# Kernel tuning notes

Hardware: AMD Instinct MI355X
Metric: run time of the kernel (lower is better)

The kernel has to match this reference:

```python
import jax, jax.numpy as jnp
import numpy as np

B, S, HID = 2, 2048, 2048
NH, NKV, HD = 16, 4, 128
GROUPS = NH // NKV
CLIP = 8.0
ROPE_THETA = 500000.0
QKV_OUT = HID + 2 * NKV * HD  # 3072
NEG = jnp.finfo(jnp.float32).min


def setup_inputs() -> dict:
    key = jax.random.key(0)
    k1, k2, k3 = jax.random.split(key, 3)
    hidden_states = jax.random.normal(k1, (B, S, HID), dtype=jnp.float32)
    position_ids = jnp.tile(jnp.arange(S, dtype=jnp.int64)[None, :], (B, 1))
    Wqkv = jax.random.normal(k2, (QKV_OUT, HID), dtype=jnp.float32) * (HID ** -0.5)
    Wout = jax.random.normal(k3, (HID, HID), dtype=jnp.float32) * (HID ** -0.5)
    return {"hidden_states": hidden_states, "position_ids": position_ids,
            "Wqkv": Wqkv, "Wout": Wout}


def _rotate_half(x):
    x1, x2 = jnp.split(x, 2, axis=-1)
    return jnp.concatenate((-x2, x1), axis=-1)


def reference(hidden_states, position_ids, Wqkv, Wout):
    b, s, _ = hidden_states.shape
    # fused QKV projection + clamp
    qkv = jnp.einsum('bsh,oh->bso', hidden_states, Wqkv)
    qkv = jnp.clip(qkv, -CLIP, CLIP)
    q, k, v = jnp.split(qkv, [HID, HID + NKV * HD], axis=2)
    q = q.reshape(b, s, NH, HD).transpose(0, 2, 1, 3)   # [b, nh, s, hd]
    k = k.reshape(b, s, NKV, HD).transpose(0, 2, 1, 3)  # [b, nkv, s, hd]
    v = v.reshape(b, s, NKV, HD).transpose(0, 2, 1, 3)
    # rotary embedding
    inv_freq = 1.0 / (ROPE_THETA ** (jnp.arange(0, HD, 2, dtype=jnp.float32) / HD))
    freqs = position_ids.astype(jnp.float32)[:, :, None] * inv_freq[None, None, :]  # [b,s,hd/2]
    emb = jnp.concatenate((freqs, freqs), axis=-1)      # [b, s, hd]
    cos = jnp.cos(emb)[:, None, :, :]                   # [b, 1, s, hd]
    sin = jnp.sin(emb)[:, None, :, :]
    q = q * cos + _rotate_half(q) * sin
    k = k * cos + _rotate_half(k) * sin
    # repeat kv heads (GQA)
    k = jnp.repeat(k, GROUPS, axis=1)  # [b, nh, s, hd]
    v = jnp.repeat(v, GROUPS, axis=1)
    # attention with additive causal mask
    scores = jnp.einsum('bhqd,bhkd->bhqk', q, k) / jnp.sqrt(jnp.float32(HD))
    causal = jnp.where(jnp.tril(jnp.ones((s, s), dtype=bool)), 0.0, NEG)
    scores = scores + causal[None, None, :, :]
    attn = jax.nn.softmax(scores.astype(jnp.float32), axis=-1).astype(q.dtype)
    out = jnp.einsum('bhqk,bhkd->bhqd', attn, v)
    out = out.transpose(0, 2, 1, 3).reshape(b, s, HID)
    return jnp.einsum('bsh,oh->bso', out, Wout)
```

## Files before the change

kernel.cpp:

```cpp
#include <hip/hip_runtime.h>
#include <stdint.h>

#define S_    2048
#define HID_  2048
#define NH_   16
#define NKV_  4
#define HD_   128

using short4x = __attribute__((ext_vector_type(4))) short;
using short8  = __attribute__((ext_vector_type(8))) short;
using floatx4 = __attribute__((ext_vector_type(4))) float;

#define NEGBIG (-3.0e38f)

__device__ __forceinline__ unsigned short f2bf(float x) {
  union { float f; unsigned u; } v; v.f = x;
  unsigned r = v.u + 0x7fffu + ((v.u >> 16) & 1u);
  return (unsigned short)(r >> 16);
}
__device__ __forceinline__ float bf2f(unsigned short b) {
  union { unsigned u; float f; } v; v.u = ((unsigned)b) << 16;
  return v.f;
}
__device__ __forceinline__ void ld_lds16(const void* g, void* l) {
  __builtin_amdgcn_global_load_lds(
      (const __attribute__((address_space(1))) unsigned*)g,
      (__attribute__((address_space(3))) unsigned*)l, 16, 0, 0);
}

__global__ void k_cvt3(const float* __restrict__ s0, unsigned short* __restrict__ d0, int n0,
                       const float* __restrict__ s1, unsigned short* __restrict__ d1, int n1,
                       const float* __restrict__ s2, unsigned short* __restrict__ d2, int n2) {
  int i = blockIdx.x * blockDim.x + threadIdx.x;
  const float* s; unsigned short* d;
  if (i < n0) { s = s0; d = d0; }
  else if (i < n0 + n1) { s = s1; d = d1; i -= n0; }
  else { s = s2; d = d2; i -= n0 + n1; if (i >= n2) return; }
  float4 v = ((const float4*)s)[i];
  union { unsigned short us[4]; uint2 u2; } u;
  u.us[0] = f2bf(v.x); u.us[1] = f2bf(v.y); u.us[2] = f2bf(v.z); u.us[3] = f2bf(v.w);
  ((uint2*)d)[i] = u.u2;
}

__global__ void k_rope2(unsigned short* __restrict__ Qb, unsigned short* __restrict__ Kb,
                        const int* __restrict__ pos, int nQ, float qscale) {
  int idx = blockIdx.x * blockDim.x + threadIdx.x;
  unsigned short* buf; int nh; float oscale;
  if (idx < nQ) { buf = Qb; nh = NH_; oscale = qscale; }
  else { buf = Kb; nh = NKV_; oscale = 1.0f; idx -= nQ; }
  int d = idx & 63;
  int h = (idx >> 6) % nh;
  int m = idx / (unsigned)(nh << 6);
  float p = (float)pos[m];
  float inv = expf(-(float)d * (13.122363377404328f / 64.0f));
  float f = p * inv;
  float cs = cosf(f), sn = sinf(f);
  size_t base = (size_t)m * (nh * HD_) + h * HD_ + d;
  float x1 = bf2f(buf[base]), x2 = bf2f(buf[base + 64]);
  buf[base]      = f2bf((x1 * cs - x2 * sn) * oscale);
  buf[base + 64] = f2bf((x2 * cs + x1 * sn) * oscale);
}

template <int EPI>
__global__ void __launch_bounds__(256)
k_gemm_bt(const unsigned short* __restrict__ A, const unsigned short* __restrict__ Bw,
          unsigned short* __restrict__ Qb, unsigned short* __restrict__ Kb,
          unsigned short* __restrict__ Vt, float* __restrict__ Of) {
  const int K = HID_;
  __shared__ __align__(16) unsigned short As[128 * 32];
  __shared__ __align__(16) unsigned short Bs[128 * 32];
  const int tid  = threadIdx.x;
  const int wave = tid >> 6, lane = tid & 63;
  const int quad = lane >> 4, l15 = lane & 15;
  const int wm = (wave >> 1) * 64, wn = (wave & 1) * 64;
  const int m0 = blockIdx.x * 128, n0 = blockIdx.y * 128;

  floatx4 acc[4][4] = {};

  const int srow = tid >> 2;
  const int scol = (tid & 3) * 8;
  const unsigned short* Ag0 = A  + (size_t)(m0 + srow)      * K + scol;
  const unsigned short* Ag1 = A  + (size_t)(m0 + 64 + srow) * K + scol;
  const unsigned short* Bg0 = Bw + (size_t)(n0 + srow)      * K + scol;
  const unsigned short* Bg1 = Bw + (size_t)(n0 + 64 + srow) * K + scol;
  unsigned short* lA0 = &As[tid * 8];
  unsigned short* lA1 = &As[2048 + tid * 8];
  unsigned short* lB0 = &Bs[tid * 8];
  unsigned short* lB1 = &Bs[2048 + tid * 8];

  for (int k0 = 0; k0 < K; k0 += 32) {
    __syncthreads();
    ld_lds16(Ag0 + k0, lA0);
    ld_lds16(Ag1 + k0, lA1);
    ld_lds16(Bg0 + k0, lB0);
    ld_lds16(Bg1 + k0, lB1);
    __syncthreads();
    short8 a[4], b[4];
#pragma unroll
    for (int i = 0; i < 4; i++) a[i] = *(const short8*)&As[(wm + i * 16 + l15) * 32 + quad * 8];
#pragma unroll
    for (int j = 0; j < 4; j++) b[j] = *(const short8*)&Bs[(wn + j * 16 + l15) * 32 + quad * 8];
#pragma unroll
    for (int i = 0; i < 4; i++)
#pragma unroll
      for (int j = 0; j < 4; j++)
        acc[i][j] = __builtin_amdgcn_mfma_f32_16x16x32_bf16(a[i], b[j], acc[i][j], 0, 0, 0);
  }

#pragma unroll
  for (int i = 0; i < 4; i++) {
#pragma unroll
    for (int j = 0; j < 4; j++) {
      const int col = n0 + wn + j * 16 + l15;
#pragma unroll
      for (int r = 0; r < 4; r++) {
        const int row = m0 + wm + i * 16 + quad * 4 + r;
        float x = acc[i][j][r];
        if (EPI == 0) {
          x = fminf(fmaxf(x, -8.0f), 8.0f);
          if (col < HID_) {
            Qb[(size_t)row * HID_ + col] = f2bf(x);
          } else if (col < HID_ + NKV_ * HD_) {
            Kb[(size_t)row * (NKV_ * HD_) + (col - HID_)] = f2bf(x);
          } else {
            int oo = col - (HID_ + NKV_ * HD_);
            int kvh = oo >> 7, d = oo & 127;
            int bb = row >> 11, ss = row & 2047;
            Vt[((size_t)((bb * NKV_ + kvh) * HD_ + d) << 11) + ss] = f2bf(x);
          }
        } else {
          Of[(size_t)row * HID_ + col] = x;
        }
      }
    }
  }
}

__global__ void __launch_bounds__(256, 2)
k_attn(const unsigned short* __restrict__ Qb, const unsigned short* __restrict__ Kb,
       const unsigned short* __restrict__ Vt, unsigned short* __restrict__ AO) {
  __shared__ __align__(16) unsigned short sm[2][16384];
  __shared__ __align__(16) unsigned short Pl[4][16][88];

  const int tid  = threadIdx.x;
  const int wave = tid >> 6, lane = tid & 63;
  const int quad = lane >> 4, l15 = lane & 15;
  const int tLow  = blockIdx.x;
  const int tHigh = 31 - tLow;
  const int q0L = tLow * 64, q0H = tHigh * 64;
  const int bh = blockIdx.y;
  const int b = bh >> 4, h = bh & 15;
  const int kvh = h >> 2;

  const int srow = tid >> 2;
  const int scolz = (((tid & 3) ^ ((tid >> 3) & 3)) * 8);
  const int qoff = ((quad ^ ((l15 >> 1) & 3)) * 8);

  {
    const unsigned short* qgL = Qb + (size_t)(b * S_ + q0L + srow) * HID_ + h * HD_ + scolz;
    const unsigned short* qgH = Qb + (size_t)(b * S_ + q0H + srow) * HID_ + h * HD_ + scolz;
#pragma unroll
    for (int i = 0; i < 4; i++) ld_lds16(qgL + i * 32, &sm[0][i * 2048 + tid * 8]);
#pragma unroll
    for (int i = 0; i < 4; i++) ld_lds16(qgH + i * 32, &sm[1][i * 2048 + tid * 8]);
  }
  __syncthreads();
  short8 qaL[4], qaH[4];
#pragma unroll
  for (int c = 0; c < 4; c++) {
    qaL[c] = *(const short8*)&sm[0][(c * 64 + wave * 16 + l15) * 32 + qoff];
    qaH[c] = *(const short8*)&sm[1][(c * 64 + wave * 16 + l15) * 32 + qoff];
  }
  __syncthreads();

  floatx4 oacL[8] = {}, oacH[8] = {};
  floatx4 oacEL = {}, oacEH = {};
  float mL = NEGBIG, mH = NEGBIG;

  const unsigned short* kgb = Kb + (size_t)b * S_ * (NKV_ * HD_) + kvh * HD_ + scolz;
  const unsigned short* vgb = Vt + (size_t)(b * NKV_ + kvh) * HD_ * S_;

  unsigned short* PlW = &Pl[wave][0][0];

  short8 ones;
#pragma unroll
  for (int i = 0; i < 8; i++) ones[i] = (short)0x3F80;

  auto stage = [&](int bufI, int j) {
    unsigned short* B = &sm[bufI][0];
    const unsigned short* kg = kgb + (size_t)(j * 64 + srow) * (NKV_ * HD_);
#pragma unroll
    for (int i = 0; i < 4; i++) ld_lds16(kg + i * 32, &B[i * 2048 + tid * 8]);
#pragma unroll
    for (int i = 0; i < 4; i++) {
      int c = i >> 1, rowd = (i & 1) * 64 + srow;
      ld_lds16(vgb + (size_t)rowd * S_ + j * 64 + c * 32 + scolz,
               &B[8192 + c * 4096 + (i & 1) * 2048 + tid * 8]);
    }
  };

  auto softmax_tile = [&](floatx4* sc, floatx4* oac, floatx4& oacE, float& m_run,
                          int q0, int j, bool diag, short8& pa0, short8& pa1) {
    if (diag) {
      const int rowq = q0 + wave * 16 + l15;
#pragma unroll
      for (int t = 0; t < 4; t++) {
        const int kb0 = j * 64 + t * 16 + quad * 4;
#pragma unroll
        for (int r = 0; r < 4; r++)
          if (kb0 + r > rowq) sc[t][r] = NEGBIG;
      }
    }
    float mx = sc[0][0];
#pragma unroll
    for (int t = 0; t < 4; t++)
#pragma unroll
      for (int r = 0; r < 4; r++) mx = fmaxf(mx, sc[t][r]);
    mx = fmaxf(mx, __shfl_xor(mx, 16));
    mx = fmaxf(mx, __shfl_xor(mx, 32));

    const float mo = m_run;
    m_run = fmaxf(mo, mx);
    if (__any(mx > mo)) {
      float alpha = __builtin_amdgcn_exp2f(mo - m_run);
      float al4[4];
#pragma unroll
      for (int r = 0; r < 4; r++) al4[r] = __shfl(alpha, quad * 4 + r, 16);
#pragma unroll
      for (int t = 0; t < 8; t++)
#pragma unroll
        for (int r = 0; r < 4; r++) oac[t][r] *= al4[r];
#pragma unroll
      for (int r = 0; r < 4; r++) oacE[r] *= al4[r];
    }
#pragma unroll
    for (int t = 0; t < 4; t++) {
      short4x pk;
#pragma unroll
      for (int r = 0; r < 4; r++)
        pk[r] = (short)f2bf(__builtin_amdgcn_exp2f(sc[t][r] - m_run));
      *(short4x*)&PlW[l15 * 88 + t * 16 + quad * 4] = pk;
    }
    pa0 = *(const short8*)&PlW[l15 * 88 + quad * 8];
    pa1 = *(const short8*)&PlW[l15 * 88 + 32 + quad * 8];
  };

  auto step_two = [&](int j, const unsigned short* Kt, const unsigned short* Vts,
                      bool diagL, bool diagH) {
    floatx4 scH[4] = {}, scL[4] = {};
#pragma unroll
    for (int t = 0; t < 4; t++)
#pragma unroll
      for (int c = 0; c < 4; c++) {
        short8 ka = *(const short8*)&Kt[c * 2048 + (t * 16 + l15) * 32 + qoff];
        scH[t] = __builtin_amdgcn_mfma_f32_16x16x32_bf16(ka, qaH[c], scH[t], 0, 0, 0);
        scL[t] = __builtin_amdgcn_mfma_f32_16x16x32_bf16(ka, qaL[c], scL[t], 0, 0, 0);
      }
    short8 paH0, paH1, paL0, paL1;
    softmax_tile(scH, oacH, oacEH, mH, q0H, j, diagH, paH0, paH1);
    softmax_tile(scL, oacL, oacEL, mL, q0L, j, diagL, paL0, paL1);
#pragma unroll
    for (int t = 0; t < 8; t++) {
      short8 vb0 = *(const short8*)&Vts[(t * 16 + l15) * 32 + qoff];
      oacH[t] = __builtin_amdgcn_mfma_f32_16x16x32_bf16(paH0, vb0, oacH[t], 0, 0, 0);
      oacL[t] = __builtin_amdgcn_mfma_f32_16x16x32_bf16(paL0, vb0, oacL[t], 0, 0, 0);
      short8 vb1 = *(const short8*)&Vts[4096 + (t * 16 + l15) * 32 + qoff];
      oacH[t] = __builtin_amdgcn_mfma_f32_16x16x32_bf16(paH1, vb1, oacH[t], 0, 0, 0);
      oacL[t] = __builtin_amdgcn_mfma_f32_16x16x32_bf16(paL1, vb1, oacL[t], 0, 0, 0);
    }
    oacEH = __builtin_amdgcn_mfma_f32_16x16x32_bf16(paH0, ones, oacEH, 0, 0, 0);
    oacEH = __builtin_amdgcn_mfma_f32_16x16x32_bf16(paH1, ones, oacEH, 0, 0, 0);
    oacEL = __builtin_amdgcn_mfma_f32_16x16x32_bf16(paL0, ones, oacEL, 0, 0, 0);
    oacEL = __builtin_amdgcn_mfma_f32_16x16x32_bf16(paL1, ones, oacEL, 0, 0, 0);
  };

  auto step_one = [&](int j, const unsigned short* Kt, const unsigned short* Vts, bool diagH) {
    floatx4 scH[4] = {};
#pragma unroll
    for (int t = 0; t < 4; t++)
#pragma unroll
      for (int c = 0; c < 4; c++) {
        short8 ka = *(const short8*)&Kt[c * 2048 + (t * 16 + l15) * 32 + qoff];
        scH[t] = __builtin_amdgcn_mfma_f32_16x16x32_bf16(ka, qaH[c], scH[t], 0, 0, 0);
      }
    short8 paH0, paH1;
    softmax_tile(scH, oacH, oacEH, mH, q0H, j, diagH, paH0, paH1);
#pragma unroll
    for (int t = 0; t < 8; t++) {
      short8 vb0 = *(const short8*)&Vts[(t * 16 + l15) * 32 + qoff];
      oacH[t] = __builtin_amdgcn_mfma_f32_16x16x32_bf16(paH0, vb0, oacH[t], 0, 0, 0);
      short8 vb1 = *(const short8*)&Vts[4096 + (t * 16 + l15) * 32 + qoff];
      oacH[t] = __builtin_amdgcn_mfma_f32_16x16x32_bf16(paH1, vb1, oacH[t], 0, 0, 0);
    }
    oacEH = __builtin_amdgcn_mfma_f32_16x16x32_bf16(paH0, ones, oacEH, 0, 0, 0);
    oacEH = __builtin_amdgcn_mfma_f32_16x16x32_bf16(paH1, ones, oacEH, 0, 0, 0);
  };

  stage(0, 0);
  int cur = 0;
  for (int j = 0; j <= tHigh; ++j) {
    __syncthreads();
    if (j < tHigh) stage(cur ^ 1, j + 1);
    const unsigned short* Kt  = &sm[cur][0];
    const unsigned short* Vts = Kt + 8192;
    if (j <= tLow) step_two(j, Kt, Vts, j == tLow, j == tHigh);
    else           step_one(j, Kt, Vts, j == tHigh);
    cur ^= 1;
  }

#pragma unroll
  for (int t = 0; t < 8; t++)
#pragma unroll
    for (int r = 0; r < 4; r++) {
      int rgL = q0L + wave * 16 + quad * 4 + r;
      int rgH = q0H + wave * 16 + quad * 4 + r;
      AO[(size_t)(b * S_ + rgL) * HID_ + h * HD_ + t * 16 + l15] = f2bf(oacL[t][r] / oacEL[r]);
      AO[(size_t)(b * S_ + rgH) * HID_ + h * HD_ + t * 16 + l15] = f2bf(oacH[t][r] / oacEH[r]);
    }
}

extern "C" void kernel_launch(void* const* d_in, const int* in_sizes, int n_in,
                              void* d_out, int out_size, void* d_ws, size_t ws_size,
                              hipStream_t stream) {
  (void)in_sizes; (void)n_in; (void)out_size; (void)ws_size;
  const float* hidden = (const float*)d_in[0];
  const int*   pos    = (const int*)d_in[1];
  const float* Wqkv   = (const float*)d_in[2];
  const float* Wout   = (const float*)d_in[3];
  float* out = (float*)d_out;

  unsigned short* ws = (unsigned short*)d_ws;
  const size_t M1 = 1024 * 1024;
  unsigned short* hb  = ws;
  unsigned short* wqb = ws + 8 * M1;
  unsigned short* wob = ws + 14 * M1;
  unsigned short* Qb  = ws + 18 * M1;
  unsigned short* Kb  = ws + 26 * M1;
  unsigned short* Vt  = ws + 28 * M1;
  unsigned short* AO  = hb;

  const float QSCL = 0.08838834764831845f * 1.4426950408889634f;
  const int nQrope = 2 * 2048 * NH_ * 64;
  const int nKrope = 2 * 2048 * NKV_ * 64;

  k_cvt3<<<18432, 256, 0, stream>>>(hidden, hb, 2097152,
                                    Wqkv, wqb, 1572864,
                                    Wout, wob, 1048576);
  k_gemm_bt<0><<<dim3(32, 24), 256, 0, stream>>>(hb, wqb, Qb, Kb, Vt, nullptr);
  k_rope2<<<(nQrope + nKrope) / 256, 256, 0, stream>>>(Qb, Kb, pos, nQrope, QSCL);
  k_attn<<<dim3(16, 32), 256, 0, stream>>>(Qb, Kb, Vt, AO);
  k_gemm_bt<1><<<dim3(32, 16), 256, 0, stream>>>(AO, wob, nullptr, nullptr, nullptr, out);
}
```

Baseline: 314.1 us.

## Replace GEMM with 256-row tiled, multi-stage pipelined, swizzled-LDS kernel

Replaces the 128x128 single-buffered bf16 GEMM with a 512-thread kernel using 256xBN tiles, a four-slot LDS ring prefetched two stages ahead, XOR-swizzled LDS addressing, workgroup-ID remapping for cache locality, and raised wave priority around the MFMA blocks. The goal is to hide global-load latency behind MFMA work, raise arithmetic intensity per tile and cut LDS bank conflicts in both projection GEMMs. The cost is a much larger LDS footprint and more registers, which limits occupancy. The hand-placed waitcnt and barrier sequencing adds synchronisation complexity, and the larger tiles give smaller grids that may leave CUs idle.

```diff
diff --git a/kernel.cpp b/kernel.cpp
--- a/kernel.cpp
+++ b/kernel.cpp
@@ -61,61 +61,108 @@
   buf[base + 64] = f2bf((x2 * cs + x1 * sn) * oscale);
 }
 
-template <int EPI>
-__global__ void __launch_bounds__(256)
-k_gemm_bt(const unsigned short* __restrict__ A, const unsigned short* __restrict__ Bw,
+template <int NREP, int EPI>
+__global__ void __launch_bounds__(512, 2)
+k_gemm256(const unsigned short* __restrict__ A, const unsigned short* __restrict__ Bw,
           unsigned short* __restrict__ Qb, unsigned short* __restrict__ Kb,
           unsigned short* __restrict__ Vt, float* __restrict__ Of) {
-  const int K = HID_;
-  __shared__ __align__(16) unsigned short As[128 * 32];
-  __shared__ __align__(16) unsigned short Bs[128 * 32];
+  constexpr int K  = HID_;
+  constexpr int NS = K / 32;
+  constexpr int BN = NREP * 64;
+  constexpr int LPS = 2 + BN / 128;
+
+  __shared__ __align__(16) unsigned short As[4][256 * 32];
+  __shared__ __align__(16) unsigned short Bs[4][BN * 32];
+
   const int tid  = threadIdx.x;
-  const int wave = tid >> 6, lane = tid & 63;
+  const int lane = tid & 63;
+  const int wid  = tid >> 6;
   const int quad = lane >> 4, l15 = lane & 15;
-  const int wm = (wave >> 1) * 64, wn = (wave & 1) * 64;
-  const int m0 = blockIdx.x * 128, n0 = blockIdx.y * 128;
-
-  floatx4 acc[4][4] = {};
-
-  const int srow = tid >> 2;
-  const int scol = (tid & 3) * 8;
-  const unsigned short* Ag0 = A  + (size_t)(m0 + srow)      * K + scol;
-  const unsigned short* Ag1 = A  + (size_t)(m0 + 64 + srow) * K + scol;
-  const unsigned short* Bg0 = Bw + (size_t)(n0 + srow)      * K + scol;
-  const unsigned short* Bg1 = Bw + (size_t)(n0 + 64 + srow) * K + scol;
-  unsigned short* lA0 = &As[tid * 8];
-  unsigned short* lA1 = &As[2048 + tid * 8];
-  unsigned short* lB0 = &Bs[tid * 8];
-  unsigned short* lB1 = &Bs[2048 + tid * 8];
-
-  for (int k0 = 0; k0 < K; k0 += 32) {
-    __syncthreads();
-    ld_lds16(Ag0 + k0, lA0);
-    ld_lds16(Ag1 + k0, lA1);
-    ld_lds16(Bg0 + k0, lB0);
-    ld_lds16(Bg1 + k0, lB1);
-    __syncthreads();
-    short8 a[4], b[4];
-#pragma unroll
-    for (int i = 0; i < 4; i++) a[i] = *(const short8*)&As[(wm + i * 16 + l15) * 32 + quad * 8];
-#pragma unroll
-    for (int j = 0; j < 4; j++) b[j] = *(const short8*)&Bs[(wn + j * 16 + l15) * 32 + quad * 8];
-#pragma unroll
-    for (int i = 0; i < 4; i++)
-#pragma unroll
-      for (int j = 0; j < 4; j++)
-        acc[i][j] = __builtin_amdgcn_mfma_f32_16x16x32_bf16(a[i], b[j], acc[i][j], 0, 0, 0);
+  const int wr = wid >> 2, wc = wid & 3;
+
+  const int gx = gridDim.x, gy = gridDim.y;
+  const int nwg = gx * gy;
+  const int lid = blockIdx.y * gx + blockIdx.x;
+  const int u = (lid & 7) * (nwg >> 3) + (lid >> 3);
+  const int by = u % gy;
+  const int bx = u / gy;
+  const int m0 = bx * 256, n0 = by * BN;
+
+  const int srow  = tid >> 2;
+  const int scolz = (((tid & 3) ^ ((tid >> 3) & 3)) * 8);
+  const int qoffz = ((quad ^ ((l15 >> 1) & 3)) * 8);
+
+  const unsigned short* Asrc = A  + (size_t)(m0 + srow) * K + scolz;
+  const unsigned short* Bsrc = Bw + (size_t)(n0 + srow) * K + scolz;
+
+  auto stageA = [&](int s) {
+    const int sl = s & 3;
+    const unsigned short* g = Asrc + s * 32;
+    ld_lds16(g, &As[sl][tid * 8]);
+    ld_lds16(g + (size_t)128 * K, &As[sl][4096 + tid * 8]);
+  };
+  auto stageB = [&](int s) {
+    const int sl = s & 3;
+    const unsigned short* g = Bsrc + s * 32;
+    ld_lds16(g, &Bs[sl][tid * 8]);
+    if (NREP == 4) ld_lds16(g + (size_t)128 * K, &Bs[sl][4096 + tid * 8]);
+  };
+
+  floatx4 acc[8][NREP] = {};
+
+  stageA(0); stageB(0); stageA(1); stageB(1);
+  asm volatile("s_waitcnt vmcnt(%0)" :: "n"(LPS) : "memory");
+  asm volatile("s_barrier" ::: "memory");
+
+  for (int s = 0; s < NS; ++s) {
+    const int sl = s & 3;
+    const bool pf = (s + 2 < NS);
+    short8 a[8], b[NREP];
+#pragma unroll
+    for (int m = 0; m < 8; ++m)
+      a[m] = *(const short8*)&As[sl][(wr * 128 + m * 16 + l15) * 32 + qoffz];
+#pragma unroll
+    for (int n = 0; n < 2; ++n)
+      b[n] = *(const short8*)&Bs[sl][(wc * (NREP * 16) + n * 16 + l15) * 32 + qoffz];
+    if (pf) stageA(s + 2);
+    if (NREP == 2 && pf) stageB(s + 2);
+    asm volatile("s_barrier" ::: "memory");
+    __builtin_amdgcn_s_setprio(1);
+#pragma unroll
+    for (int m = 0; m < 8; ++m)
+#pragma unroll
+      for (int n = 0; n < 2; ++n)
+        acc[m][n] = __builtin_amdgcn_mfma_f32_16x16x32_bf16(a[m], b[n], acc[m][n], 0, 0, 0);
+    __builtin_amdgcn_s_setprio(0);
+    asm volatile("s_barrier" ::: "memory");
+    if (NREP == 4) {
+#pragma unroll
+      for (int n = 2; n < 4; ++n)
+        b[n] = *(const short8*)&Bs[sl][(wc * 64 + n * 16 + l15) * 32 + qoffz];
+      if (pf) stageB(s + 2);
+      asm volatile("s_barrier" ::: "memory");
+      __builtin_amdgcn_s_setprio(1);
+#pragma unroll
+      for (int m = 0; m < 8; ++m)
+#pragma unroll
+        for (int n = 2; n < 4; ++n)
+          acc[m][n] = __builtin_amdgcn_mfma_f32_16x16x32_bf16(a[m], b[n], acc[m][n], 0, 0, 0);
+      __builtin_amdgcn_s_setprio(0);
+    }
+    if (pf) asm volatile("s_waitcnt vmcnt(%0)" :: "n"(LPS) : "memory");
+    else    asm volatile("s_waitcnt vmcnt(0)" ::: "memory");
+    asm volatile("s_barrier" ::: "memory");
   }
 
 #pragma unroll
-  for (int i = 0; i < 4; i++) {
-#pragma unroll
-    for (int j = 0; j < 4; j++) {
-      const int col = n0 + wn + j * 16 + l15;
-#pragma unroll
-      for (int r = 0; r < 4; r++) {
-        const int row = m0 + wm + i * 16 + quad * 4 + r;
-        float x = acc[i][j][r];
+  for (int m = 0; m < 8; ++m) {
+#pragma unroll
+    for (int n = 0; n < NREP; ++n) {
+      const int col = n0 + wc * (NREP * 16) + n * 16 + l15;
+#pragma unroll
+      for (int r = 0; r < 4; ++r) {
+        const int row = m0 + wr * 128 + m * 16 + quad * 4 + r;
+        float x = acc[m][n][r];
         if (EPI == 0) {
           x = fminf(fmaxf(x, -8.0f), 8.0f);
           if (col < HID_) {
@@ -346,8 +393,8 @@
   k_cvt3<<<18432, 256, 0, stream>>>(hidden, hb, 2097152,
                                     Wqkv, wqb, 1572864,
                                     Wout, wob, 1048576);
-  k_gemm_bt<0><<<dim3(32, 24), 256, 0, stream>>>(hb, wqb, Qb, Kb, Vt, nullptr);
+  k_gemm256<4, 0><<<dim3(16, 12), 512, 0, stream>>>(hb, wqb, Qb, Kb, Vt, nullptr);
   k_rope2<<<(nQrope + nKrope) / 256, 256, 0, stream>>>(Qb, Kb, pos, nQrope, QSCL);
   k_attn<<<dim3(16, 32), 256, 0, stream>>>(Qb, Kb, Vt, AO);
-  k_gemm_bt<1><<<dim3(32, 16), 256, 0, stream>>>(AO, wob, nullptr, nullptr, nullptr, out);
-}
+  k_gemm256<2, 1><<<dim3(16, 16), 512, 0, stream>>>(AO, wob, nullptr, nullptr, nullptr, out);
+}
```

Result: slower. 335.0 us (+6.7%).

## Replace GEMM with 8-wave double-buffered pipelined kernel using swizzled LDS

Applied to the files above, without the earlier changes.

Both projection GEMMs now use a new 512-thread kernel with 256xBN tiles, a K-step of 64, double-buffered LDS, and async global-to-LDS loads interleaved with MFMA phases using manual barriers and vmcnt waits. It adds an XOR swizzle on the LDS layout to avoid bank conflicts, a workgroup-id remap for cache locality, and s_setprio around MFMA bursts. The goal is to hide memory latency and raise MFMA utilization compared with the single-buffered 128x128 kernel that synchronized twice per 32-wide K step. In exchange it uses much more LDS and fewer blocks (192 and 256), and the hand-counted vmcnt values make correctness fragile.

```diff
diff --git a/kernel.cpp b/kernel.cpp
--- a/kernel.cpp
+++ b/kernel.cpp
@@ -27,6 +27,9 @@
       (const __attribute__((address_space(1))) unsigned*)g,
       (__attribute__((address_space(3))) unsigned*)l, 16, 0, 0);
 }
+
+#define BAR()  asm volatile("s_barrier" ::: "memory")
+#define WLDS() asm volatile("s_waitcnt lgkmcnt(0)" ::: "memory")
 
 __global__ void k_cvt3(const float* __restrict__ s0, unsigned short* __restrict__ d0, int n0,
                        const float* __restrict__ s1, unsigned short* __restrict__ d1, int n1,
@@ -61,61 +64,147 @@
   buf[base + 64] = f2bf((x2 * cs + x1 * sn) * oscale);
 }
 
-template <int EPI>
-__global__ void __launch_bounds__(256)
-k_gemm_bt(const unsigned short* __restrict__ A, const unsigned short* __restrict__ Bw,
-          unsigned short* __restrict__ Qb, unsigned short* __restrict__ Kb,
-          unsigned short* __restrict__ Vt, float* __restrict__ Of) {
-  const int K = HID_;
-  __shared__ __align__(16) unsigned short As[128 * 32];
-  __shared__ __align__(16) unsigned short Bs[128 * 32];
+template <int NREP, int EPI>
+__global__ void __launch_bounds__(512, 2)
+k_gemm8p(const unsigned short* __restrict__ A, const unsigned short* __restrict__ Bw,
+         unsigned short* __restrict__ Qb, unsigned short* __restrict__ Kb,
+         unsigned short* __restrict__ Vt, float* __restrict__ Of) {
+  constexpr int K  = HID_;
+  constexpr int NT = K / 64;
+  constexpr int BN = NREP * 64;
+
+  __shared__ __align__(16) unsigned short As[2][256 * 64];
+  __shared__ __align__(16) unsigned short Bs[2][BN * 64];
+
   const int tid  = threadIdx.x;
-  const int wave = tid >> 6, lane = tid & 63;
+  const int lane = tid & 63, wave = tid >> 6;
   const int quad = lane >> 4, l15 = lane & 15;
-  const int wm = (wave >> 1) * 64, wn = (wave & 1) * 64;
-  const int m0 = blockIdx.x * 128, n0 = blockIdx.y * 128;
-
-  floatx4 acc[4][4] = {};
-
-  const int srow = tid >> 2;
-  const int scol = (tid & 3) * 8;
-  const unsigned short* Ag0 = A  + (size_t)(m0 + srow)      * K + scol;
-  const unsigned short* Ag1 = A  + (size_t)(m0 + 64 + srow) * K + scol;
-  const unsigned short* Bg0 = Bw + (size_t)(n0 + srow)      * K + scol;
-  const unsigned short* Bg1 = Bw + (size_t)(n0 + 64 + srow) * K + scol;
-  unsigned short* lA0 = &As[tid * 8];
-  unsigned short* lA1 = &As[2048 + tid * 8];
-  unsigned short* lB0 = &Bs[tid * 8];
-  unsigned short* lB1 = &Bs[2048 + tid * 8];
-
-  for (int k0 = 0; k0 < K; k0 += 32) {
-    __syncthreads();
-    ld_lds16(Ag0 + k0, lA0);
-    ld_lds16(Ag1 + k0, lA1);
-    ld_lds16(Bg0 + k0, lB0);
-    ld_lds16(Bg1 + k0, lB1);
-    __syncthreads();
-    short8 a[4], b[4];
-#pragma unroll
-    for (int i = 0; i < 4; i++) a[i] = *(const short8*)&As[(wm + i * 16 + l15) * 32 + quad * 8];
-#pragma unroll
-    for (int j = 0; j < 4; j++) b[j] = *(const short8*)&Bs[(wn + j * 16 + l15) * 32 + quad * 8];
-#pragma unroll
-    for (int i = 0; i < 4; i++)
-#pragma unroll
-      for (int j = 0; j < 4; j++)
-        acc[i][j] = __builtin_amdgcn_mfma_f32_16x16x32_bf16(a[i], b[j], acc[i][j], 0, 0, 0);
+  const int wr = wave >> 2, wc = wave & 3;
+
+  const int gx = gridDim.x, gy = gridDim.y;
+  const int nwg = gx * gy;
+  const int lid = blockIdx.y * gx + blockIdx.x;
+  const int u = (lid & 7) * (nwg >> 3) + (lid >> 3);
+  const int by = u % gy, bx = u / gy;
+  const int m0 = bx * 256, n0 = by * BN;
+
+  const int scol = ((((tid >> 2) & 1) ^ ((tid >> 3) & 1)) * 32)
+                 + (((tid & 3) ^ ((tid >> 4) & 3)) * 8);
+  const int srow = tid >> 3;
+  const unsigned short* Ag = A  + (size_t)(m0 + srow) * K + scol;
+  const unsigned short* Bg = Bw + (size_t)(n0 + srow) * K + scol;
+
+  const int rks0 = (l15 & 1) * 32;
+  const int rks1 = rks0 ^ 32;
+  const int rsl  = (quad ^ ((l15 >> 1) & 3)) * 8;
+
+  auto stageA = [&](int t, int half) {
+    const int d = t & 1;
+    const unsigned short* g = Ag + (size_t)half * 128 * K + t * 64;
+    ld_lds16(g,                  &As[d][(half * 128) * 64 + tid * 8]);
+    ld_lds16(g + (size_t)64 * K, &As[d][(half * 128 + 64) * 64 + tid * 8]);
+  };
+  auto stageB = [&](int t, int half) {
+    const int d = t & 1;
+    const unsigned short* g = Bg + (size_t)half * 128 * K + t * 64;
+    ld_lds16(g,                  &Bs[d][(half * 128) * 64 + tid * 8]);
+    ld_lds16(g + (size_t)64 * K, &Bs[d][(half * 128 + 64) * 64 + tid * 8]);
+  };
+
+  floatx4 acc[8][NREP] = {};
+
+  auto ldA = [&](short8* a, int d, int mh) {
+#pragma unroll
+    for (int m = 0; m < 4; ++m) {
+      const int row = (mh * 4 + m) * 32 + wr * 16 + l15;
+      a[m * 2 + 0] = *(const short8*)&As[d][row * 64 + rks0 + rsl];
+      a[m * 2 + 1] = *(const short8*)&As[d][row * 64 + rks1 + rsl];
+    }
+  };
+  auto ldB = [&](short8* b, int d, int nh) {
+#pragma unroll
+    for (int n = 0; n < 2; ++n) {
+      const int row = (nh * 2 + n) * 64 + wc * 16 + l15;
+      b[n * 2 + 0] = *(const short8*)&Bs[d][row * 64 + rks0 + rsl];
+      b[n * 2 + 1] = *(const short8*)&Bs[d][row * 64 + rks1 + rsl];
+    }
+  };
+  auto mmac = [&](const short8* a, const short8* b, int mh, int nh) {
+    __builtin_amdgcn_s_setprio(1);
+#pragma unroll
+    for (int m = 0; m < 4; ++m)
+#pragma unroll
+      for (int n = 0; n < 2; ++n)
+#pragma unroll
+        for (int ks = 0; ks < 2; ++ks)
+          acc[mh * 4 + m][nh * 2 + n] = __builtin_amdgcn_mfma_f32_16x16x32_bf16(
+              a[m * 2 + ks], b[n * 2 + ks], acc[mh * 4 + m][nh * 2 + n], 0, 0, 0);
+    __builtin_amdgcn_s_setprio(0);
+  };
+
+  short8 a[8], b0[4], b1[4];
+
+  if (NREP == 4) {
+    stageA(0, 0); stageA(0, 1); stageB(0, 0); stageB(0, 1);
+    asm volatile("s_waitcnt vmcnt(4)" ::: "memory");
+    stageA(1, 0); stageB(1, 0); stageB(1, 1);
+    asm volatile("s_waitcnt vmcnt(6)" ::: "memory");
+    BAR();
+    for (int t = 0; t < NT; ++t) {
+      const int d = t & 1;
+      ldA(a, d, 0); ldB(b0, d, 0);
+      if (t + 1 < NT) stageA(t + 1, 1);
+      BAR(); WLDS();
+      mmac(a, b0, 0, 0);
+      BAR();
+      ldB(b1, d, 1);
+      if (t + 2 < NT) stageA(t + 2, 0);
+      BAR(); WLDS();
+      mmac(a, b1, 0, 1);
+      BAR();
+      ldA(a, d, 1);
+      if (t + 2 < NT) stageB(t + 2, 0);
+      BAR(); WLDS();
+      mmac(a, b1, 1, 1);
+      BAR();
+      if (t + 2 < NT) stageB(t + 2, 1);
+      mmac(a, b0, 1, 0);
+      if (t + 2 < NT) asm volatile("s_waitcnt vmcnt(6)" ::: "memory");
+      else            asm volatile("s_waitcnt vmcnt(0)" ::: "memory");
+      BAR();
+    }
+  } else {
+    stageA(0, 0); stageA(0, 1); stageB(0, 0);
+    asm volatile("s_waitcnt vmcnt(2)" ::: "memory");
+    stageA(1, 0); stageB(1, 0);
+    asm volatile("s_waitcnt vmcnt(4)" ::: "memory");
+    BAR();
+    for (int t = 0; t < NT; ++t) {
+      const int d = t & 1;
+      ldA(a, d, 0); ldB(b0, d, 0);
+      if (t + 1 < NT) stageA(t + 1, 1);
+      BAR(); WLDS();
+      mmac(a, b0, 0, 0);
+      BAR();
+      ldA(a, d, 1);
+      if (t + 2 < NT) { stageA(t + 2, 0); stageB(t + 2, 0); }
+      BAR(); WLDS();
+      mmac(a, b0, 1, 0);
+      if (t + 2 < NT) asm volatile("s_waitcnt vmcnt(4)" ::: "memory");
+      else            asm volatile("s_waitcnt vmcnt(0)" ::: "memory");
+      BAR();
+    }
   }
 
 #pragma unroll
-  for (int i = 0; i < 4; i++) {
-#pragma unroll
-    for (int j = 0; j < 4; j++) {
-      const int col = n0 + wn + j * 16 + l15;
-#pragma unroll
-      for (int r = 0; r < 4; r++) {
-        const int row = m0 + wm + i * 16 + quad * 4 + r;
-        float x = acc[i][j][r];
+  for (int mf = 0; mf < 8; ++mf) {
+#pragma unroll
+    for (int nf = 0; nf < NREP; ++nf) {
+      const int col = n0 + nf * 64 + wc * 16 + l15;
+#pragma unroll
+      for (int r = 0; r < 4; ++r) {
+        const int row = m0 + mf * 32 + wr * 16 + quad * 4 + r;
+        float x = acc[mf][nf][r];
         if (EPI == 0) {
           x = fminf(fmaxf(x, -8.0f), 8.0f);
           if (col < HID_) {
@@ -124,9 +213,9 @@
             Kb[(size_t)row * (NKV_ * HD_) + (col - HID_)] = f2bf(x);
           } else {
             int oo = col - (HID_ + NKV_ * HD_);
-            int kvh = oo >> 7, d = oo & 127;
+            int kvh = oo >> 7, d2 = oo & 127;
             int bb = row >> 11, ss = row & 2047;
-            Vt[((size_t)((bb * NKV_ + kvh) * HD_ + d) << 11) + ss] = f2bf(x);
+            Vt[((size_t)((bb * NKV_ + kvh) * HD_ + d2) << 11) + ss] = f2bf(x);
           }
         } else {
           Of[(size_t)row * HID_ + col] = x;
@@ -346,8 +435,8 @@
   k_cvt3<<<18432, 256, 0, stream>>>(hidden, hb, 2097152,
                                     Wqkv, wqb, 1572864,
                                     Wout, wob, 1048576);
-  k_gemm_bt<0><<<dim3(32, 24), 256, 0, stream>>>(hb, wqb, Qb, Kb, Vt, nullptr);
+  k_gemm8p<4, 0><<<dim3(16, 12), 512, 0, stream>>>(hb, wqb, Qb, Kb, Vt, nullptr);
   k_rope2<<<(nQrope + nKrope) / 256, 256, 0, stream>>>(Qb, Kb, pos, nQrope, QSCL);
   k_attn<<<dim3(16, 32), 256, 0, stream>>>(Qb, Kb, Vt, AO);
-  k_gemm_bt<1><<<dim3(32, 16), 256, 0, stream>>>(AO, wob, nullptr, nullptr, nullptr, out);
-}
+  k_gemm8p<2, 1><<<dim3(16, 16), 512, 0, stream>>>(AO, wob, nullptr, nullptr, nullptr, out);
+}
```

Result: slower. 338.7 us (+7.8%).

## Fuse RoPE into QKV GEMM epilogue and defer softmax rescale by threshold

Applied to the files above, without the earlier changes.

The separate rotary-embedding kernel is removed and RoPE plus the Q scale are applied in the QKV GEMM epilogue. Each wave's clamped accumulators are exchanged through shared memory so that partner halves (d and d+64) can be rotated together. Q/K tiles are now written once, which avoids a full read-modify-write pass over the Q and K buffers and one kernel launch. Separately, the attention kernel now only rescales the running max when the new max exceeds the old one by more than 8 in log2 units, which skips most rescale passes. This lazy rescaling relies on the bounded clamped inputs to keep the unrescaled exponentials within fp32 range.

```diff
diff --git a/kernel.cpp b/kernel.cpp
--- a/kernel.cpp
+++ b/kernel.cpp
@@ -12,6 +12,7 @@
 using floatx4 = __attribute__((ext_vector_type(4))) float;
 
 #define NEGBIG (-3.0e38f)
+#define QSCL_  (0.08838834764831845f * 1.4426950408889634f)
 
 __device__ __forceinline__ unsigned short f2bf(float x) {
   union { float f; unsigned u; } v; v.f = x;
@@ -42,33 +43,16 @@
   ((uint2*)d)[i] = u.u2;
 }
 
-__global__ void k_rope2(unsigned short* __restrict__ Qb, unsigned short* __restrict__ Kb,
-                        const int* __restrict__ pos, int nQ, float qscale) {
-  int idx = blockIdx.x * blockDim.x + threadIdx.x;
-  unsigned short* buf; int nh; float oscale;
-  if (idx < nQ) { buf = Qb; nh = NH_; oscale = qscale; }
-  else { buf = Kb; nh = NKV_; oscale = 1.0f; idx -= nQ; }
-  int d = idx & 63;
-  int h = (idx >> 6) % nh;
-  int m = idx / (unsigned)(nh << 6);
-  float p = (float)pos[m];
-  float inv = expf(-(float)d * (13.122363377404328f / 64.0f));
-  float f = p * inv;
-  float cs = cosf(f), sn = sinf(f);
-  size_t base = (size_t)m * (nh * HD_) + h * HD_ + d;
-  float x1 = bf2f(buf[base]), x2 = bf2f(buf[base + 64]);
-  buf[base]      = f2bf((x1 * cs - x2 * sn) * oscale);
-  buf[base + 64] = f2bf((x2 * cs + x1 * sn) * oscale);
-}
-
 template <int EPI>
 __global__ void __launch_bounds__(256)
 k_gemm_bt(const unsigned short* __restrict__ A, const unsigned short* __restrict__ Bw,
           unsigned short* __restrict__ Qb, unsigned short* __restrict__ Kb,
-          unsigned short* __restrict__ Vt, float* __restrict__ Of) {
+          unsigned short* __restrict__ Vt, float* __restrict__ Of,
+          const int* __restrict__ pos) {
   const int K = HID_;
-  __shared__ __align__(16) unsigned short As[128 * 32];
-  __shared__ __align__(16) unsigned short Bs[128 * 32];
+  __shared__ __align__(16) unsigned short smg[8192];
+  unsigned short* As = smg;
+  unsigned short* Bs = smg + 4096;
   const int tid  = threadIdx.x;
   const int wave = tid >> 6, lane = tid & 63;
   const int quad = lane >> 4, l15 = lane & 15;
@@ -107,30 +91,75 @@
         acc[i][j] = __builtin_amdgcn_mfma_f32_16x16x32_bf16(a[i], b[j], acc[i][j], 0, 0, 0);
   }
 
+  if (EPI == 1) {
+#pragma unroll
+    for (int i = 0; i < 4; i++)
+#pragma unroll
+      for (int j = 0; j < 4; j++) {
+        const int col = n0 + wn + j * 16 + l15;
+#pragma unroll
+        for (int r = 0; r < 4; r++) {
+          const int row = m0 + wm + i * 16 + quad * 4 + r;
+          Of[(size_t)row * HID_ + col] = acc[i][j][r];
+        }
+      }
+    return;
+  }
+
+  if (n0 >= HID_ + NKV_ * HD_) {
+#pragma unroll
+    for (int i = 0; i < 4; i++)
+#pragma unroll
+      for (int j = 0; j < 4; j++) {
+        const int col = n0 + wn + j * 16 + l15;
+        const int oo = col - (HID_ + NKV_ * HD_);
+        const int kvh = oo >> 7, d = oo & 127;
+#pragma unroll
+        for (int r = 0; r < 4; r++) {
+          const int row = m0 + wm + i * 16 + quad * 4 + r;
+          float x = fminf(fmaxf(acc[i][j][r], -8.0f), 8.0f);
+          int bb = row >> 11, ss = row & 2047;
+          Vt[((size_t)((bb * NKV_ + kvh) * HD_ + d) << 11) + ss] = f2bf(x);
+        }
+      }
+    return;
+  }
+
+  const float oscale = (n0 < HID_) ? QSCL_ : 1.0f;
+  float* X = (float*)smg;
+  float inv4[4];
+#pragma unroll
+  for (int j = 0; j < 4; j++)
+    inv4[j] = expf(-(float)(j * 16 + l15) * (13.122363377404328f / 64.0f));
+
 #pragma unroll
   for (int i = 0; i < 4; i++) {
+    floatx4 accC[4];
+    __syncthreads();
 #pragma unroll
     for (int j = 0; j < 4; j++) {
+      floatx4 c;
+#pragma unroll
+      for (int r = 0; r < 4; r++) c[r] = fminf(fmaxf(acc[i][j][r], -8.0f), 8.0f);
+      accC[j] = c;
+      *(floatx4*)&X[wave * 1024 + j * 256 + lane * 4] = c;
+    }
+    __syncthreads();
+    const int4 p4 = *(const int4*)&pos[m0 + wm + i * 16 + quad * 4];
+#pragma unroll
+    for (int j = 0; j < 4; j++) {
+      const floatx4 pr = *(const floatx4*)&X[(wave ^ 1) * 1024 + j * 256 + lane * 4];
       const int col = n0 + wn + j * 16 + l15;
 #pragma unroll
       for (int r = 0; r < 4; r++) {
         const int row = m0 + wm + i * 16 + quad * 4 + r;
-        float x = acc[i][j][r];
-        if (EPI == 0) {
-          x = fminf(fmaxf(x, -8.0f), 8.0f);
-          if (col < HID_) {
-            Qb[(size_t)row * HID_ + col] = f2bf(x);
-          } else if (col < HID_ + NKV_ * HD_) {
-            Kb[(size_t)row * (NKV_ * HD_) + (col - HID_)] = f2bf(x);
-          } else {
-            int oo = col - (HID_ + NKV_ * HD_);
-            int kvh = oo >> 7, d = oo & 127;
-            int bb = row >> 11, ss = row & 2047;
-            Vt[((size_t)((bb * NKV_ + kvh) * HD_ + d) << 11) + ss] = f2bf(x);
-          }
-        } else {
-          Of[(size_t)row * HID_ + col] = x;
-        }
+        const float f = (float)((&p4.x)[r]) * inv4[j];
+        const float cs = cosf(f), sn = sinf(f);
+        const float x = accC[j][r], y = pr[r];
+        float o = (wn == 0) ? (x * cs - y * sn) : (x * cs + y * sn);
+        o *= oscale;
+        if (col < HID_) Qb[(size_t)row * HID_ + col] = f2bf(o);
+        else            Kb[(size_t)row * (NKV_ * HD_) + (col - HID_)] = f2bf(o);
       }
     }
   }
@@ -220,8 +249,8 @@
     mx = fmaxf(mx, __shfl_xor(mx, 32));
 
     const float mo = m_run;
-    m_run = fmaxf(mo, mx);
-    if (__any(mx > mo)) {
+    if (__any(mx > mo + 8.0f)) {
+      m_run = fmaxf(mo, mx);
       float alpha = __builtin_amdgcn_exp2f(mo - m_run);
       float al4[4];
 #pragma unroll
@@ -339,15 +368,10 @@
   unsigned short* Vt  = ws + 28 * M1;
   unsigned short* AO  = hb;
 
-  const float QSCL = 0.08838834764831845f * 1.4426950408889634f;
-  const int nQrope = 2 * 2048 * NH_ * 64;
-  const int nKrope = 2 * 2048 * NKV_ * 64;
-
   k_cvt3<<<18432, 256, 0, stream>>>(hidden, hb, 2097152,
                                     Wqkv, wqb, 1572864,
                                     Wout, wob, 1048576);
-  k_gemm_bt<0><<<dim3(32, 24), 256, 0, stream>>>(hb, wqb, Qb, Kb, Vt, nullptr);
-  k_rope2<<<(nQrope + nKrope) / 256, 256, 0, stream>>>(Qb, Kb, pos, nQrope, QSCL);
+  k_gemm_bt<0><<<dim3(32, 24), 256, 0, stream>>>(hb, wqb, Qb, Kb, Vt, nullptr, pos);
   k_attn<<<dim3(16, 32), 256, 0, stream>>>(Qb, Kb, Vt, AO);
-  k_gemm_bt<1><<<dim3(32, 16), 256, 0, stream>>>(AO, wob, nullptr, nullptr, nullptr, out);
-}
+  k_gemm_bt<1><<<dim3(32, 16), 256, 0, stream>>>(AO, wob, nullptr, nullptr, nullptr, out, nullptr);
+}
```

Result: slower. 988.2 us (+214.6%).
